# Optimization experiments

Hardware: AMD Instinct MI355X
Metric: run time of the kernel (lower is better)

## Reference

```python
import jax, jax.numpy as jnp
import numpy as np

B, H, S, D = 2, 16, 2048, 128
SPARSITY = 0.1
NEG = -1.0e9


def local_mask(seq_len: int) -> jnp.ndarray:
    # window_size = max(1, int(seq_len * sparsity)); row i keeps cols [i-w//2, i+w//2]
    w = max(1, int(seq_len * SPARSITY))
    half = w // 2
    idx = jnp.arange(seq_len)
    diff = idx[None, :] - idx[:, None]  # j - i
    return ((diff >= -half) & (diff <= half)).astype(jnp.float32)


def setup_inputs() -> dict:
    key = jax.random.key(0)
    kq, kk, kv = jax.random.split(key, 3)
    return {
        "query": jax.random.normal(kq, (B, H, S, D), dtype=jnp.float32),
        "key": jax.random.normal(kk, (B, H, S, D), dtype=jnp.float32),
        "value": jax.random.normal(kv, (B, H, S, D), dtype=jnp.float32),
    }


def reference(query, key, value):
    head_dim = query.shape[-1]
    seq_len_k = key.shape[2]
    m = local_mask(seq_len_k)[None, None]  # [1,1,S,S]
    scores = jnp.einsum("bhqd,bhkd->bhqk", query, key) / jnp.sqrt(
        jnp.asarray(head_dim, query.dtype)
    )
    scores = scores * m + (1.0 - m) * NEG
    probs = jax.nn.softmax(scores, axis=-1)
    context = jnp.einsum("bhqk,bhkd->bhqd", probs, value)
    return context, probs
```

## Files before the change

kernel.cpp:

```cpp
#include <hip/hip_runtime.h>
#include <math.h>


namespace {
constexpr int Sc = 2048, Dc = 128;
constexpr int HALFW = 102;
constexpr float SCALE = 0.08838834764831845f;
constexpr int TQ  = 32;
constexpr int CT  = 256;
constexpr int KST = 136;
constexpr int VST = 132;
constexpr int PTS = 36;
constexpr int OFF_KBUF = 0;
constexpr int OFF_PST  = 34816;
constexpr int OFF_QS   = 34816;
constexpr int OFF_RED  = 34816 + 36864;
constexpr int LDS_TOTAL = OFF_RED + 512 + 128 + 128;
}

typedef __bf16 bf16x8 __attribute__((ext_vector_type(8)));
typedef float  f32x16 __attribute__((ext_vector_type(16)));
typedef float  fx4    __attribute__((ext_vector_type(4)));

__device__ __forceinline__ unsigned short f2bf(float f) {
    unsigned u = __float_as_uint(f);
    u += 0x7fffu + ((u >> 16) & 1u);
    return (unsigned short)(u >> 16);
}

__global__ __launch_bounds__(256, 2) void sparse_attn_mfma(
    const float* __restrict__ Q, const float* __restrict__ K,
    const float* __restrict__ V, float* __restrict__ ctx,
    float* __restrict__ probs)
{
    __shared__ __align__(16) unsigned char smem[LDS_TOTAL];
    unsigned short* Ks   = (unsigned short*)(smem + OFF_KBUF);
    float*          Vsf  = (float*)(smem + OFF_KBUF);
    float*          Ps_t = (float*)(smem + OFF_PST);
    unsigned short* Qs   = (unsigned short*)(smem + OFF_QS);
    float (*red)[4]      = (float(*)[4])(smem + OFF_RED);
    float* rowM          = (float*)(smem + OFF_RED + 512);
    float* rowSinv       = (float*)(smem + OFF_RED + 512 + 128);

    const int tid  = threadIdx.x;
    const int lane = tid & 63;
    const int w    = tid >> 6;
    const int lo   = lane & 31;
    const int hi   = lane >> 5;

    const int wid = (blockIdx.x & 7) * 256 + (blockIdx.x >> 3);
    const int bh  = wid >> 6;
    const int qt  = wid & 63;
    const int i0  = qt * TQ;
    const int js0 = max(0, i0 - HALFW);
    const int jend = min(js0 + CT, Sc);

    const size_t rowbase = (size_t)bh * Sc;
    float* probsBase = probs + (rowbase + i0) * (size_t)Sc;

    {
        const int headN = js0 & 3;
        const int tailN = (4 - (jend & 3)) & 3;
        const int hn = headN + tailN;
        if (hn == 4) {
            int r = tid >> 2, s = tid & 3;
            if (r < TQ) {
                int col = (s < headN) ? (js0 - headN + s) : (jend + s - headN);
                __builtin_nontemporal_store(0.0f, probsBase + (size_t)r * Sc + col);
            }
        } else if (hn == 2) {
            int r = tid >> 1, s = tid & 1;
            if (r < TQ) {
                int col = (s < headN) ? (js0 - headN + s) : (jend + s - headN);
                __builtin_nontemporal_store(0.0f, probsBase + (size_t)r * Sc + col);
            }
        }
        const int leftQ   = (js0 - headN) >> 2;
        const int rightQ0 = (jend + tailN) >> 2;
        const fx4 z4 = {0.f, 0.f, 0.f, 0.f};
        for (int r = 0; r < TQ; ++r) {
            fx4* p4 = (fx4*)(probsBase + (size_t)r * Sc);
            for (int c = tid; c < leftQ; c += 256)
                __builtin_nontemporal_store(z4, p4 + c);
            for (int c = rightQ0 + tid; c < Sc / 4; c += 256)
                __builtin_nontemporal_store(z4, p4 + c);
        }
    }

    {
        const float4* Q4 = (const float4*)(Q + (rowbase + i0) * Dc);
        #pragma unroll
        for (int it = 0; it < 4; ++it) {
            int idx = tid + 256 * it;
            int r = idx >> 5, d4 = idx & 31;
            float4 q4 = Q4[r * 32 + d4];
            ushort4 b;
            b.x = f2bf(q4.x); b.y = f2bf(q4.y); b.z = f2bf(q4.z); b.w = f2bf(q4.w);
            *(ushort4*)&Qs[r * KST + d4 * 4] = b;
        }
    }

    const float4* K4 = (const float4*)(K + rowbase * Dc);
    const float4* V4 = (const float4*)(V + rowbase * Dc);

    f32x16 accE[2];
    #pragma unroll
    for (int ch = 0; ch < 2; ++ch) {
        #pragma unroll
        for (int it = 0; it < 16; ++it) {
            int idx = tid + 256 * it;
            int r = idx >> 5, d4 = idx & 31;
            int jn = js0 + ch * 128 + r;
            if (jn > Sc - 1) jn = Sc - 1;
            float4 k4 = K4[(size_t)jn * 32 + d4];
            ushort4 b;
            b.x = f2bf(k4.x); b.y = f2bf(k4.y); b.z = f2bf(k4.z); b.w = f2bf(k4.w);
            *(ushort4*)&Ks[r * KST + d4 * 4] = b;
        }
        __syncthreads();
        f32x16 acc;
        #pragma unroll
        for (int i = 0; i < 16; ++i) acc[i] = 0.0f;
        const unsigned short* qrow = &Qs[lo * KST + hi * 8];
        const unsigned short* krow = &Ks[(w * 32 + lo) * KST + hi * 8];
        #pragma unroll
        for (int dk = 0; dk < 8; ++dk) {
            bf16x8 a = *(const bf16x8*)(qrow + dk * 16);
            bf16x8 b = *(const bf16x8*)(krow + dk * 16);
            acc = __builtin_amdgcn_mfma_f32_32x32x16_bf16(a, b, acc, 0, 0, 0);
        }
        accE[ch] = acc;
        __syncthreads();
    }

    const int cg0 = js0 + w * 32 + lo;
    {
        float mred[16];
        #pragma unroll
        for (int i = 0; i < 16; ++i) {
            int rl = (i & 3) + 8 * (i >> 2) + 4 * hi;
            int rg = i0 + rl;
            float m = -3.0e38f;
            #pragma unroll
            for (int ch = 0; ch < 2; ++ch) {
                int cg = cg0 + ch * 128;
                bool valid = (cg < Sc) & (cg >= rg - HALFW) & (cg <= rg + HALFW);
                float sv = valid ? accE[ch][i] * SCALE : -3.0e38f;
                accE[ch][i] = sv;
                m = fmaxf(m, sv);
            }
            mred[i] = m;
        }
        #pragma unroll
        for (int mk = 1; mk < 32; mk <<= 1) {
            #pragma unroll
            for (int i = 0; i < 16; ++i)
                mred[i] = fmaxf(mred[i], __shfl_xor(mred[i], mk, 64));
        }
        if (lo == 0) {
            #pragma unroll
            for (int i = 0; i < 16; ++i) {
                int rl = (i & 3) + 8 * (i >> 2) + 4 * hi;
                red[rl][w] = mred[i];
            }
        }
    }
    __syncthreads();
    if (tid < 128) {
        int rr = tid >> 2, sl = tid & 3;
        float v = red[rr][sl];
        v = fmaxf(v, __shfl_xor(v, 1, 64));
        v = fmaxf(v, __shfl_xor(v, 2, 64));
        if (sl == 0) rowM[rr] = v;
    }
    __syncthreads();

    {
        float sred[16];
        #pragma unroll
        for (int i = 0; i < 16; ++i) {
            int rl = (i & 3) + 8 * (i >> 2) + 4 * hi;
            float rm = rowM[rl];
            float e0 = __expf(accE[0][i] - rm);
            float e1 = __expf(accE[1][i] - rm);
            accE[0][i] = e0; accE[1][i] = e1;
            sred[i] = e0 + e1;
        }
        #pragma unroll
        for (int mk = 1; mk < 32; mk <<= 1) {
            #pragma unroll
            for (int i = 0; i < 16; ++i)
                sred[i] += __shfl_xor(sred[i], mk, 64);
        }
        if (lo == 0) {
            #pragma unroll
            for (int i = 0; i < 16; ++i) {
                int rl = (i & 3) + 8 * (i >> 2) + 4 * hi;
                red[rl][w] = sred[i];
            }
        }
    }
    __syncthreads();
    if (tid < 128) {
        int rr = tid >> 2, sl = tid & 3;
        float v = red[rr][sl];
        v += __shfl_xor(v, 1, 64);
        v += __shfl_xor(v, 2, 64);
        if (sl == 0) rowSinv[rr] = 1.0f / v;
    }
    __syncthreads();

    #pragma unroll
    for (int i = 0; i < 16; ++i) {
        int rl = (i & 3) + 8 * (i >> 2) + 4 * hi;
        float inv = rowSinv[rl];
        float* prow = probsBase + (size_t)rl * Sc;
        #pragma unroll
        for (int ch = 0; ch < 2; ++ch) {
            int cg = cg0 + ch * 128;
            float p = accE[ch][i] * inv;
            Ps_t[(cg - js0) * PTS + rl] = p;
            if (cg < Sc) __builtin_nontemporal_store(p, prow + cg);
        }
    }
    __syncthreads();

    const int kp  = lane & 3;
    const int dgq = (lane >> 2) & 1;
    const int rg  = lane >> 3;
    fx4 o[4][4];
    #pragma unroll
    for (int c = 0; c < 4; ++c)
        #pragma unroll
        for (int j = 0; j < 4; ++j) o[c][j] = (fx4){0.f, 0.f, 0.f, 0.f};

    #pragma unroll
    for (int ch4 = 0; ch4 < 4; ++ch4) {
        #pragma unroll
        for (int it = 0; it < 8; ++it) {
            int idx = tid + 256 * it;
            int r = idx >> 5, d4 = idx & 31;
            int jn = js0 + ch4 * 64 + r;
            if (jn > Sc - 1) jn = Sc - 1;
            float4 v4g = V4[(size_t)jn * 32 + d4];
            *(float4*)&Vsf[r * VST + d4 * 4] = v4g;
        }
        __syncthreads();
        const float* Pbase = &Ps_t[(ch4 * 64) * PTS + 4 * rg];
        const float* Vbase = &Vsf[w * 32 + dgq * 16];
        #pragma unroll 4
        for (int kk = 0; kk < 16; ++kk) {
            int k = 4 * kk + kp;
            fx4 p4 = *(const fx4*)(Pbase + k * PTS);
            const float* vr = Vbase + k * VST;
            fx4 v0 = *(const fx4*)(vr);
            fx4 v1 = *(const fx4*)(vr + 4);
            fx4 v2 = *(const fx4*)(vr + 8);
            fx4 v3 = *(const fx4*)(vr + 12);
            #pragma unroll
            for (int c = 0; c < 4; ++c) {
                float pc = p4[c];
                o[c][0] += v0 * pc;
                o[c][1] += v1 * pc;
                o[c][2] += v2 * pc;
                o[c][3] += v3 * pc;
            }
        }
        __syncthreads();
    }

    #pragma unroll
    for (int c = 0; c < 4; ++c) {
        #pragma unroll
        for (int j = 0; j < 4; ++j) {
            fx4 t = o[c][j];
            #pragma unroll
            for (int comp = 0; comp < 4; ++comp) {
                float s = t[comp];
                s += __shfl_xor(s, 1, 64);
                s += __shfl_xor(s, 2, 64);
                t[comp] = s;
            }
            o[c][j] = t;
        }
    }
    if (kp == 0) {
        #pragma unroll
        for (int c = 0; c < 4; ++c) {
            float* crow = ctx + (rowbase + i0 + 4 * rg + c) * (size_t)Dc
                        + w * 32 + dgq * 16;
            #pragma unroll
            for (int j = 0; j < 4; ++j)
                __builtin_nontemporal_store(o[c][j], (fx4*)crow + j);
        }
    }
}

extern "C" void kernel_launch(void* const* d_in, const int* in_sizes, int n_in,
                              void* d_out, int out_size, void* d_ws, size_t ws_size,
                              hipStream_t stream) {
    const float* Q = (const float*)d_in[0];
    const float* K = (const float*)d_in[1];
    const float* V = (const float*)d_in[2];
    float* out   = (float*)d_out;
    float* ctx   = out;
    float* probs = out + (size_t)2 * 16 * 2048 * 128;

    dim3 grid(2 * 16 * (Sc / TQ));
    dim3 block(256);
    sparse_attn_mfma<<<grid, block, 0, stream>>>(Q, K, V, ctx, probs);
}
```

Before: 688.7 us.

## Use bf16 MFMA for PV product with swizzled LDS and move zero-fill after compute

Replaces the scalar fp32 P·V accumulation with bf16 MFMA 32x32x16, staging V transposed in bf16 and P in bf16 with XOR-swizzled LDS layouts. K/Q LDS layouts also become swizzled, and the LDS footprint shrinks so launch bounds can request 3 blocks per CU. The large zero-fill of the probs row outside the window now runs at the end of the kernel rather than at the start. This lowers FMA and LDS traffic in the PV stage, at the cost of bf16 rounding of probabilities and V.

```diff
diff --git a/kernel.cpp b/kernel.cpp
--- a/kernel.cpp
+++ b/kernel.cpp
@@ -8,13 +8,12 @@
 constexpr float SCALE = 0.08838834764831845f;
 constexpr int TQ  = 32;
 constexpr int CT  = 256;
-constexpr int KST = 136;
-constexpr int VST = 132;
-constexpr int PTS = 36;
+constexpr int KSB = 272;
+constexpr int PSB = 512;
 constexpr int OFF_KBUF = 0;
-constexpr int OFF_PST  = 34816;
+constexpr int OFF_PS   = 34816;
 constexpr int OFF_QS   = 34816;
-constexpr int OFF_RED  = 34816 + 36864;
+constexpr int OFF_RED  = 34816 + 16384;
 constexpr int LDS_TOTAL = OFF_RED + 512 + 128 + 128;
 }
 
@@ -28,16 +27,12 @@
     return (unsigned short)(u >> 16);
 }
 
-__global__ __launch_bounds__(256, 2) void sparse_attn_mfma(
+__global__ __launch_bounds__(256, 3) void sparse_attn_mfma(
     const float* __restrict__ Q, const float* __restrict__ K,
     const float* __restrict__ V, float* __restrict__ ctx,
     float* __restrict__ probs)
 {
     __shared__ __align__(16) unsigned char smem[LDS_TOTAL];
-    unsigned short* Ks   = (unsigned short*)(smem + OFF_KBUF);
-    float*          Vsf  = (float*)(smem + OFF_KBUF);
-    float*          Ps_t = (float*)(smem + OFF_PST);
-    unsigned short* Qs   = (unsigned short*)(smem + OFF_QS);
     float (*red)[4]      = (float(*)[4])(smem + OFF_RED);
     float* rowM          = (float*)(smem + OFF_RED + 512);
     float* rowSinv       = (float*)(smem + OFF_RED + 512 + 128);
@@ -57,6 +52,216 @@
 
     const size_t rowbase = (size_t)bh * Sc;
     float* probsBase = probs + (rowbase + i0) * (size_t)Sc;
+
+    {
+        const float4* Q4 = (const float4*)(Q + (rowbase + i0) * Dc);
+        #pragma unroll
+        for (int it = 0; it < 4; ++it) {
+            int idx = tid + 256 * it;
+            int r = idx >> 5, d4 = idx & 31;
+            float4 q4 = Q4[r * 32 + d4];
+            ushort4 b;
+            b.x = f2bf(q4.x); b.y = f2bf(q4.y); b.z = f2bf(q4.z); b.w = f2bf(q4.w);
+            *(ushort4*)(smem + OFF_QS + ((r * KSB + d4 * 8) ^ ((r >> 3) << 4))) = b;
+        }
+    }
+
+    const float4* K4 = (const float4*)(K + rowbase * Dc);
+    const float4* V4 = (const float4*)(V + rowbase * Dc);
+
+    auto stageV = [&](int h) {
+        const int dq  = tid & 31;
+        const int kb8 = tid >> 5;
+        const int kbase = js0 + 128 * h;
+        #pragma unroll
+        for (int s = 0; s < 4; ++s) {
+            int kb = kb8 + 8 * s;
+            int k4 = kbase + kb * 4;
+            float4 a0 = V4[(size_t)min(k4 + 0, Sc - 1) * 32 + dq];
+            float4 a1 = V4[(size_t)min(k4 + 1, Sc - 1) * 32 + dq];
+            float4 a2 = V4[(size_t)min(k4 + 2, Sc - 1) * 32 + dq];
+            float4 a3 = V4[(size_t)min(k4 + 3, Sc - 1) * 32 + dq];
+            const float* f0 = (const float*)&a0;
+            const float* f1 = (const float*)&a1;
+            const float* f2 = (const float*)&a2;
+            const float* f3 = (const float*)&a3;
+            #pragma unroll
+            for (int m = 0; m < 4; ++m) {
+                ushort4 bb;
+                bb.x = f2bf(f0[m]); bb.y = f2bf(f1[m]);
+                bb.z = f2bf(f2[m]); bb.w = f2bf(f3[m]);
+                int d = 4 * dq + m;
+                *(ushort4*)(smem + OFF_KBUF +
+                            ((d * KSB + 8 * kb) ^ (((d >> 3) & 7) << 4))) = bb;
+            }
+        }
+    };
+
+    f32x16 accE[2];
+    {
+        const int qswz = (lo >> 3) << 4;
+        const int rk   = w * 32 + lo;
+        const int kswz = ((rk >> 3) & 7) << 4;
+        #pragma unroll
+        for (int ch = 0; ch < 2; ++ch) {
+            #pragma unroll
+            for (int it = 0; it < 16; ++it) {
+                int idx = tid + 256 * it;
+                int r = idx >> 5, d4 = idx & 31;
+                int jn = js0 + ch * 128 + r;
+                if (jn > Sc - 1) jn = Sc - 1;
+                float4 k4 = K4[(size_t)jn * 32 + d4];
+                ushort4 b;
+                b.x = f2bf(k4.x); b.y = f2bf(k4.y); b.z = f2bf(k4.z); b.w = f2bf(k4.w);
+                *(ushort4*)(smem + OFF_KBUF +
+                            ((r * KSB + d4 * 8) ^ (((r >> 3) & 7) << 4))) = b;
+            }
+            __syncthreads();
+            f32x16 acc;
+            #pragma unroll
+            for (int i = 0; i < 16; ++i) acc[i] = 0.0f;
+            #pragma unroll
+            for (int dk = 0; dk < 8; ++dk) {
+                bf16x8 a = *(const bf16x8*)(smem + OFF_QS +
+                            ((lo * KSB + hi * 16 + dk * 32) ^ qswz));
+                bf16x8 b = *(const bf16x8*)(smem + OFF_KBUF +
+                            ((rk * KSB + hi * 16 + dk * 32) ^ kswz));
+                acc = __builtin_amdgcn_mfma_f32_32x32x16_bf16(a, b, acc, 0, 0, 0);
+            }
+            accE[ch] = acc;
+            __syncthreads();
+        }
+    }
+
+    stageV(0);
+
+    const int cg0 = js0 + w * 32 + lo;
+    {
+        float mred[16];
+        #pragma unroll
+        for (int i = 0; i < 16; ++i) {
+            int rl = (i & 3) + 8 * (i >> 2) + 4 * hi;
+            int rg = i0 + rl;
+            float m = -3.0e38f;
+            #pragma unroll
+            for (int ch = 0; ch < 2; ++ch) {
+                int cg = cg0 + ch * 128;
+                bool valid = (cg < Sc) & (cg >= rg - HALFW) & (cg <= rg + HALFW);
+                float sv = valid ? accE[ch][i] * SCALE : -3.0e38f;
+                accE[ch][i] = sv;
+                m = fmaxf(m, sv);
+            }
+            mred[i] = m;
+        }
+        #pragma unroll
+        for (int mk = 1; mk < 32; mk <<= 1) {
+            #pragma unroll
+            for (int i = 0; i < 16; ++i)
+                mred[i] = fmaxf(mred[i], __shfl_xor(mred[i], mk, 64));
+        }
+        if (lo == 0) {
+            #pragma unroll
+            for (int i = 0; i < 16; ++i) {
+                int rl = (i & 3) + 8 * (i >> 2) + 4 * hi;
+                red[rl][w] = mred[i];
+            }
+        }
+    }
+    __syncthreads();
+    if (tid < 128) {
+        int rr = tid >> 2, sl = tid & 3;
+        float v = red[rr][sl];
+        v = fmaxf(v, __shfl_xor(v, 1, 64));
+        v = fmaxf(v, __shfl_xor(v, 2, 64));
+        if (sl == 0) rowM[rr] = v;
+    }
+    __syncthreads();
+
+    {
+        float sred[16];
+        #pragma unroll
+        for (int i = 0; i < 16; ++i) {
+            int rl = (i & 3) + 8 * (i >> 2) + 4 * hi;
+            float rm = rowM[rl];
+            float e0 = __expf(accE[0][i] - rm);
+            float e1 = __expf(accE[1][i] - rm);
+            accE[0][i] = e0; accE[1][i] = e1;
+            sred[i] = e0 + e1;
+        }
+        #pragma unroll
+        for (int mk = 1; mk < 32; mk <<= 1) {
+            #pragma unroll
+            for (int i = 0; i < 16; ++i)
+                sred[i] += __shfl_xor(sred[i], mk, 64);
+        }
+        if (lo == 0) {
+            #pragma unroll
+            for (int i = 0; i < 16; ++i) {
+                int rl = (i & 3) + 8 * (i >> 2) + 4 * hi;
+                red[rl][w] = sred[i];
+            }
+        }
+    }
+    __syncthreads();
+    if (tid < 128) {
+        int rr = tid >> 2, sl = tid & 3;
+        float v = red[rr][sl];
+        v += __shfl_xor(v, 1, 64);
+        v += __shfl_xor(v, 2, 64);
+        if (sl == 0) rowSinv[rr] = 1.0f / v;
+    }
+    __syncthreads();
+
+    #pragma unroll
+    for (int i = 0; i < 16; ++i) {
+        int rl = (i & 3) + 8 * (i >> 2) + 4 * hi;
+        float inv = rowSinv[rl];
+        float* prow = probsBase + (size_t)rl * Sc;
+        #pragma unroll
+        for (int ch = 0; ch < 2; ++ch) {
+            int cg = cg0 + ch * 128;
+            float p = accE[ch][i] * inv;
+            int kix = cg - js0;
+            *(unsigned short*)(smem + OFF_PS +
+                ((rl * PSB + 2 * kix) ^ ((rl & 7) << 4))) = f2bf(p);
+            if (cg < Sc) __builtin_nontemporal_store(p, prow + cg);
+        }
+    }
+    __syncthreads();
+
+    f32x16 oacc;
+    #pragma unroll
+    for (int i = 0; i < 16; ++i) oacc[i] = 0.0f;
+    const int dloc = 32 * w + lo;
+    const int vswz = ((dloc >> 3) & 7) << 4;
+    const int pswz = (lo & 7) << 4;
+
+    #pragma unroll
+    for (int ks = 0; ks < 8; ++ks) {
+        bf16x8 pa = *(const bf16x8*)(smem + OFF_PS +
+                    ((lo * PSB + 32 * ks + 16 * hi) ^ pswz));
+        bf16x8 vb = *(const bf16x8*)(smem + OFF_KBUF +
+                    ((dloc * KSB + 32 * ks + 16 * hi) ^ vswz));
+        oacc = __builtin_amdgcn_mfma_f32_32x32x16_bf16(pa, vb, oacc, 0, 0, 0);
+    }
+    __syncthreads();
+    stageV(1);
+    __syncthreads();
+    #pragma unroll
+    for (int ks = 0; ks < 8; ++ks) {
+        bf16x8 pa = *(const bf16x8*)(smem + OFF_PS +
+                    ((lo * PSB + 256 + 32 * ks + 16 * hi) ^ pswz));
+        bf16x8 vb = *(const bf16x8*)(smem + OFF_KBUF +
+                    ((dloc * KSB + 32 * ks + 16 * hi) ^ vswz));
+        oacc = __builtin_amdgcn_mfma_f32_32x32x16_bf16(pa, vb, oacc, 0, 0, 0);
+    }
+
+    #pragma unroll
+    for (int i = 0; i < 16; ++i) {
+        int rl = (i & 3) + 8 * (i >> 2) + 4 * hi;
+        __builtin_nontemporal_store(oacc[i],
+            ctx + (rowbase + i0 + rl) * (size_t)Dc + dloc);
+    }
 
     {
         const int headN = js0 & 3;
@@ -86,214 +291,6 @@
                 __builtin_nontemporal_store(z4, p4 + c);
         }
     }
-
-    {
-        const float4* Q4 = (const float4*)(Q + (rowbase + i0) * Dc);
-        #pragma unroll
-        for (int it = 0; it < 4; ++it) {
-            int idx = tid + 256 * it;
-            int r = idx >> 5, d4 = idx & 31;
-            float4 q4 = Q4[r * 32 + d4];
-            ushort4 b;
-            b.x = f2bf(q4.x); b.y = f2bf(q4.y); b.z = f2bf(q4.z); b.w = f2bf(q4.w);
-            *(ushort4*)&Qs[r * KST + d4 * 4] = b;
-        }
-    }
-
-    const float4* K4 = (const float4*)(K + rowbase * Dc);
-    const float4* V4 = (const float4*)(V + rowbase * Dc);
-
-    f32x16 accE[2];
-    #pragma unroll
-    for (int ch = 0; ch < 2; ++ch) {
-        #pragma unroll
-        for (int it = 0; it < 16; ++it) {
-            int idx = tid + 256 * it;
-            int r = idx >> 5, d4 = idx & 31;
-            int jn = js0 + ch * 128 + r;
-            if (jn > Sc - 1) jn = Sc - 1;
-            float4 k4 = K4[(size_t)jn * 32 + d4];
-            ushort4 b;
-            b.x = f2bf(k4.x); b.y = f2bf(k4.y); b.z = f2bf(k4.z); b.w = f2bf(k4.w);
-            *(ushort4*)&Ks[r * KST + d4 * 4] = b;
-        }
-        __syncthreads();
-        f32x16 acc;
-        #pragma unroll
-        for (int i = 0; i < 16; ++i) acc[i] = 0.0f;
-        const unsigned short* qrow = &Qs[lo * KST + hi * 8];
-        const unsigned short* krow = &Ks[(w * 32 + lo) * KST + hi * 8];
-        #pragma unroll
-        for (int dk = 0; dk < 8; ++dk) {
-            bf16x8 a = *(const bf16x8*)(qrow + dk * 16);
-            bf16x8 b = *(const bf16x8*)(krow + dk * 16);
-            acc = __builtin_amdgcn_mfma_f32_32x32x16_bf16(a, b, acc, 0, 0, 0);
-        }
-        accE[ch] = acc;
-        __syncthreads();
-    }
-
-    const int cg0 = js0 + w * 32 + lo;
-    {
-        float mred[16];
-        #pragma unroll
-        for (int i = 0; i < 16; ++i) {
-            int rl = (i & 3) + 8 * (i >> 2) + 4 * hi;
-            int rg = i0 + rl;
-            float m = -3.0e38f;
-            #pragma unroll
-            for (int ch = 0; ch < 2; ++ch) {
-                int cg = cg0 + ch * 128;
-                bool valid = (cg < Sc) & (cg >= rg - HALFW) & (cg <= rg + HALFW);
-                float sv = valid ? accE[ch][i] * SCALE : -3.0e38f;
-                accE[ch][i] = sv;
-                m = fmaxf(m, sv);
-            }
-            mred[i] = m;
-        }
-        #pragma unroll
-        for (int mk = 1; mk < 32; mk <<= 1) {
-            #pragma unroll
-            for (int i = 0; i < 16; ++i)
-                mred[i] = fmaxf(mred[i], __shfl_xor(mred[i], mk, 64));
-        }
-        if (lo == 0) {
-            #pragma unroll
-            for (int i = 0; i < 16; ++i) {
-                int rl = (i & 3) + 8 * (i >> 2) + 4 * hi;
-                red[rl][w] = mred[i];
-            }
-        }
-    }
-    __syncthreads();
-    if (tid < 128) {
-        int rr = tid >> 2, sl = tid & 3;
-        float v = red[rr][sl];
-        v = fmaxf(v, __shfl_xor(v, 1, 64));
-        v = fmaxf(v, __shfl_xor(v, 2, 64));
-        if (sl == 0) rowM[rr] = v;
-    }
-    __syncthreads();
-
-    {
-        float sred[16];
-        #pragma unroll
-        for (int i = 0; i < 16; ++i) {
-            int rl = (i & 3) + 8 * (i >> 2) + 4 * hi;
-            float rm = rowM[rl];
-            float e0 = __expf(accE[0][i] - rm);
-            float e1 = __expf(accE[1][i] - rm);
-            accE[0][i] = e0; accE[1][i] = e1;
-            sred[i] = e0 + e1;
-        }
-        #pragma unroll
-        for (int mk = 1; mk < 32; mk <<= 1) {
-            #pragma unroll
-            for (int i = 0; i < 16; ++i)
-                sred[i] += __shfl_xor(sred[i], mk, 64);
-        }
-        if (lo == 0) {
-            #pragma unroll
-            for (int i = 0; i < 16; ++i) {
-                int rl = (i & 3) + 8 * (i >> 2) + 4 * hi;
-                red[rl][w] = sred[i];
-            }
-        }
-    }
-    __syncthreads();
-    if (tid < 128) {
-        int rr = tid >> 2, sl = tid & 3;
-        float v = red[rr][sl];
-        v += __shfl_xor(v, 1, 64);
-        v += __shfl_xor(v, 2, 64);
-        if (sl == 0) rowSinv[rr] = 1.0f / v;
-    }
-    __syncthreads();
-
-    #pragma unroll
-    for (int i = 0; i < 16; ++i) {
-        int rl = (i & 3) + 8 * (i >> 2) + 4 * hi;
-        float inv = rowSinv[rl];
-        float* prow = probsBase + (size_t)rl * Sc;
-        #pragma unroll
-        for (int ch = 0; ch < 2; ++ch) {
-            int cg = cg0 + ch * 128;
-            float p = accE[ch][i] * inv;
-            Ps_t[(cg - js0) * PTS + rl] = p;
-            if (cg < Sc) __builtin_nontemporal_store(p, prow + cg);
-        }
-    }
-    __syncthreads();
-
-    const int kp  = lane & 3;
-    const int dgq = (lane >> 2) & 1;
-    const int rg  = lane >> 3;
-    fx4 o[4][4];
-    #pragma unroll
-    for (int c = 0; c < 4; ++c)
-        #pragma unroll
-        for (int j = 0; j < 4; ++j) o[c][j] = (fx4){0.f, 0.f, 0.f, 0.f};
-
-    #pragma unroll
-    for (int ch4 = 0; ch4 < 4; ++ch4) {
-        #pragma unroll
-        for (int it = 0; it < 8; ++it) {
-            int idx = tid + 256 * it;
-            int r = idx >> 5, d4 = idx & 31;
-            int jn = js0 + ch4 * 64 + r;
-            if (jn > Sc - 1) jn = Sc - 1;
-            float4 v4g = V4[(size_t)jn * 32 + d4];
-            *(float4*)&Vsf[r * VST + d4 * 4] = v4g;
-        }
-        __syncthreads();
-        const float* Pbase = &Ps_t[(ch4 * 64) * PTS + 4 * rg];
-        const float* Vbase = &Vsf[w * 32 + dgq * 16];
-        #pragma unroll 4
-        for (int kk = 0; kk < 16; ++kk) {
-            int k = 4 * kk + kp;
-            fx4 p4 = *(const fx4*)(Pbase + k * PTS);
-            const float* vr = Vbase + k * VST;
-            fx4 v0 = *(const fx4*)(vr);
-            fx4 v1 = *(const fx4*)(vr + 4);
-            fx4 v2 = *(const fx4*)(vr + 8);
-            fx4 v3 = *(const fx4*)(vr + 12);
-            #pragma unroll
-            for (int c = 0; c < 4; ++c) {
-                float pc = p4[c];
-                o[c][0] += v0 * pc;
-                o[c][1] += v1 * pc;
-                o[c][2] += v2 * pc;
-                o[c][3] += v3 * pc;
-            }
-        }
-        __syncthreads();
-    }
-
-    #pragma unroll
-    for (int c = 0; c < 4; ++c) {
-        #pragma unroll
-        for (int j = 0; j < 4; ++j) {
-            fx4 t = o[c][j];
-            #pragma unroll
-            for (int comp = 0; comp < 4; ++comp) {
-                float s = t[comp];
-                s += __shfl_xor(s, 1, 64);
-                s += __shfl_xor(s, 2, 64);
-                t[comp] = s;
-            }
-            o[c][j] = t;
-        }
-    }
-    if (kp == 0) {
-        #pragma unroll
-        for (int c = 0; c < 4; ++c) {
-            float* crow = ctx + (rowbase + i0 + 4 * rg + c) * (size_t)Dc
-                        + w * 32 + dgq * 16;
-            #pragma unroll
-            for (int j = 0; j < 4; ++j)
-                __builtin_nontemporal_store(o[c][j], (fx4*)crow + j);
-        }
-    }
 }
 
 extern "C" void kernel_launch(void* const* d_in, const int* in_sizes, int n_in,
```

New measurement: 682.0 us. Within noise of the previous version (-1.0%).
